# Performance work log

Hardware: AMD Instinct MI355X
Metric: run time of the kernel (lower is better)

The kernel has to match this reference:

```python
import jax, jax.numpy as jnp
import numpy as np

DIM = 512
QK_DIM = 128
B, N = 4, 4096
LN_EPS = 1e-5


def setup_inputs() -> dict:
    key = jax.random.key(0)
    ks = jax.random.split(key, 4)
    x = jax.random.normal(ks[0], (B, N, DIM), dtype=jnp.float32)
    ln_w = jnp.ones((DIM,), jnp.float32)
    ln_b = jnp.zeros((DIM,), jnp.float32)
    # Linear(dim -> qk_dim): torch default kaiming-uniform; small uniform is fine
    lim = 1.0 / np.sqrt(DIM)
    w_qk = jax.random.uniform(ks[1], (QK_DIM, DIM), jnp.float32, -lim, lim)
    b_qk = jax.random.uniform(ks[2], (QK_DIM,), jnp.float32, -lim, lim)
    # OffsetScale: gamma ~ N(0, 0.02), beta = 0, heads=2 (q, k)
    gamma = 0.02 * jax.random.normal(ks[3], (2, QK_DIM), jnp.float32)
    beta = jnp.zeros((2, QK_DIM), jnp.float32)
    return {"x": x, "ln_w": ln_w, "ln_b": ln_b, "w_qk": w_qk, "b_qk": b_qk, "gamma": gamma, "beta": beta}


def reference(x, ln_w, ln_b, w_qk, b_qk, gamma, beta):
    n = x.shape[-2]
    # LayerNorm over last dim
    mu = jnp.mean(x, axis=-1, keepdims=True)
    var = jnp.mean((x - mu) ** 2, axis=-1, keepdims=True)
    normed = (x - mu) * jax.lax.rsqrt(var + LN_EPS) * ln_w + ln_b
    # Linear + SiLU -> [b, n, qk_dim]
    qk = jax.nn.silu(jnp.einsum('bnd,ed->bne', normed, w_qk) + b_qk)
    # OffsetScale, heads=2 -> q, k
    q = qk * gamma[0] + beta[0]
    k = qk * gamma[1] + beta[1]
    # relu^2 row-normalized attention, [b, n, n]
    sim = jnp.einsum('bid,bjd->bij', q, k) / jnp.sqrt(jnp.float32(n))
    attn = jnp.square(jax.nn.relu(sim))
    attn = attn / (jnp.sum(attn, axis=-1, keepdims=True) + 1e-6)
    return attn
```

## Files before the change

kernel.cpp:

```cpp
#include <hip/hip_runtime.h>

#define DIM 512
#define QKD 128
#define BATCH 4
#define SEQ 4096

typedef __attribute__((ext_vector_type(8)))  _Float16 f16x8;
typedef __attribute__((ext_vector_type(4)))  _Float16 f16x4;
typedef __attribute__((ext_vector_type(4)))  float    f32x4;
typedef __attribute__((ext_vector_type(16))) float    f32x16;

__global__ __launch_bounds__(256) void wcvt_kernel(
    const float* __restrict__ w, _Float16* __restrict__ w16)
{
    const int i = (blockIdx.x * 256 + threadIdx.x) * 4;
    const float4 v = *(const float4*)(w + i);
    f16x4 o;
    o[0] = (_Float16)v.x; o[1] = (_Float16)v.y;
    o[2] = (_Float16)v.z; o[3] = (_Float16)v.w;
    *(f16x4*)(w16 + i) = o;
}

__global__ __launch_bounds__(256) void ln_qk_kernel(
    const float* __restrict__ x,
    const float* __restrict__ ln_w,
    const float* __restrict__ ln_b,
    const _Float16* __restrict__ w16,
    const float* __restrict__ b_qk,
    const float* __restrict__ gamma,
    const float* __restrict__ beta,
    _Float16* __restrict__ q_h,
    _Float16* __restrict__ k_h)
{
    __shared__ _Float16 As[32][520];
    const int tid  = threadIdx.x;
    const int wave = tid >> 6;
    const int lane = tid & 63;
    const int row0 = blockIdx.x * 32;

    float lw[8], lb[8];
    {
        const float4* w4 = (const float4*)ln_w;
        const float4* b4 = (const float4*)ln_b;
        float4 w0 = w4[lane * 2], w1 = w4[lane * 2 + 1];
        float4 b0 = b4[lane * 2], b1 = b4[lane * 2 + 1];
        lw[0]=w0.x; lw[1]=w0.y; lw[2]=w0.z; lw[3]=w0.w;
        lw[4]=w1.x; lw[5]=w1.y; lw[6]=w1.z; lw[7]=w1.w;
        lb[0]=b0.x; lb[1]=b0.y; lb[2]=b0.z; lb[3]=b0.w;
        lb[4]=b1.x; lb[5]=b1.y; lb[6]=b1.z; lb[7]=b1.w;
    }

    for (int rr = 0; rr < 8; ++rr) {
        const int r = wave * 8 + rr;
        const float4* xr = (const float4*)(x + (size_t)(row0 + r) * DIM);
        float4 v0 = xr[lane * 2], v1 = xr[lane * 2 + 1];
        float xv[8] = {v0.x, v0.y, v0.z, v0.w, v1.x, v1.y, v1.z, v1.w};
        float s = 0.f, s2 = 0.f;
#pragma unroll
        for (int j = 0; j < 8; ++j) { s += xv[j]; s2 = fmaf(xv[j], xv[j], s2); }
#pragma unroll
        for (int off = 32; off > 0; off >>= 1) {
            s  += __shfl_xor(s,  off);
            s2 += __shfl_xor(s2, off);
        }
        const float mu   = s * (1.f / DIM);
        const float var  = s2 * (1.f / DIM) - mu * mu;
        const float rstd = rsqrtf(var + 1e-5f);
        f16x8 hh;
#pragma unroll
        for (int j = 0; j < 8; ++j)
            hh[j] = (_Float16)(fmaf((xv[j] - mu) * rstd, lw[j], lb[j]));
        *(f16x8*)&As[r][lane * 8] = hh;
    }
    __syncthreads();

    const int mtile = wave & 1;
    const int nbase = (wave >> 1) * 64;
    const int lcol  = lane & 15;
    const int quad  = lane >> 4;

    f32x4 acc[4];
#pragma unroll
    for (int nt = 0; nt < 4; ++nt) acc[nt] = (f32x4){0.f, 0.f, 0.f, 0.f};

    const _Float16* arow = &As[mtile * 16 + lcol][quad * 8];
#pragma unroll 4
    for (int kc = 0; kc < 16; ++kc) {
        const f16x8 af = *(const f16x8*)(arow + kc * 32);
#pragma unroll
        for (int nt = 0; nt < 4; ++nt) {
            const int e = nbase + nt * 16 + lcol;
            const f16x8 bfr = *(const f16x8*)(w16 + (size_t)e * DIM + kc * 32 + quad * 8);
            acc[nt] = __builtin_amdgcn_mfma_f32_16x16x32_f16(af, bfr, acc[nt], 0, 0, 0);
        }
    }

    const size_t gbase = (size_t)blockIdx.x * 4096;
#pragma unroll
    for (int nt = 0; nt < 4; ++nt) {
        const int e = nbase + nt * 16 + lcol;
        const float bq  = b_qk[e];
        const float g0  = gamma[e]       * 0.125f;
        const float g1  = gamma[QKD + e] * 0.125f;
        const float be0 = beta[e]        * 0.125f;
        const float be1 = beta[QKD + e]  * 0.125f;
        const int eo = (e >> 3) * 256 + (e & 7);
#pragma unroll
        for (int reg = 0; reg < 4; ++reg) {
            const int m  = mtile * 16 + quad * 4 + reg;
            const float v   = acc[nt][reg] + bq;
            const float sil = v / (1.f + __expf(-v));
            const size_t off = gbase + (size_t)(eo + m * 8);
            q_h[off] = (_Float16)fmaf(sil, g0, be0);
            k_h[off] = (_Float16)fmaf(sil, g1, be1);
        }
    }
}

__global__ __launch_bounds__(256, 4) void rowsum_kernel(
    const _Float16* __restrict__ q_h,
    const _Float16* __restrict__ k_h,
    float* __restrict__ rsum)
{
    const int l     = blockIdx.x;
    const int batch = (l & 7) >> 1;
    const int chunk = ((l & 1) << 1) | ((l >> 3) & 1);
    const int tile  = l >> 4;
    const int r0    = tile * 32;

    const int wid  = threadIdx.x >> 6;
    const int lane = threadIdx.x & 63;
    const int n    = lane & 31;
    const int h    = lane >> 5;

    const _Float16* qb = q_h + (size_t)(batch * 128 + tile) * 4096;
    f16x8 aq[8];
#pragma unroll
    for (int kc = 0; kc < 8; ++kc)
        aq[kc] = *(const f16x8*)(qb + kc * 512 + lane * 8);

    const _Float16* kb0 = k_h + (size_t)(batch * 128 + chunk * 32 + wid) * 4096
                              + lane * 8;

    __shared__ float partial[4][32];

    float rs[16];
#pragma unroll
    for (int r = 0; r < 16; ++r) rs[r] = 0.f;

#pragma unroll 2
    for (int ct = 0; ct < 8; ++ct) {
        const _Float16* cb = kb0 + (size_t)(ct * 4) * 4096;
        f16x8 bf[8];
#pragma unroll
        for (int kc = 0; kc < 8; ++kc) bf[kc] = *(const f16x8*)(cb + kc * 512);

        f32x16 acc;
#pragma unroll
        for (int r = 0; r < 16; ++r) acc[r] = 0.f;
        __builtin_amdgcn_s_setprio(1);
#pragma unroll
        for (int kc = 0; kc < 8; ++kc)
            acc = __builtin_amdgcn_mfma_f32_32x32x16_f16(aq[kc], bf[kc], acc, 0, 0, 0);
        __builtin_amdgcn_s_setprio(0);
#pragma unroll
        for (int r = 0; r < 16; ++r) {
            const float t = fmaxf(acc[r], 0.f);
            rs[r] = fmaf(t, t, rs[r]);
        }
    }

#pragma unroll
    for (int r = 0; r < 16; ++r) {
        float v = rs[r];
        v += __shfl_xor(v, 1);
        v += __shfl_xor(v, 2);
        v += __shfl_xor(v, 4);
        v += __shfl_xor(v, 8);
        v += __shfl_xor(v, 16);
        if (n == 0) partial[wid][(r & 3) + 8 * (r >> 2) + 4 * h] = v;
    }
    __syncthreads();
    if (threadIdx.x < 32) {
        const float t = partial[0][threadIdx.x] + partial[1][threadIdx.x]
                      + partial[2][threadIdx.x] + partial[3][threadIdx.x];
        rsum[((size_t)batch * 4 + chunk) * SEQ + r0 + threadIdx.x] = t;
    }
}

__global__ __launch_bounds__(256, 4) void attn_norm_kernel(
    const _Float16* __restrict__ q_h,
    const _Float16* __restrict__ k_h,
    const float* __restrict__ rsum,
    float* __restrict__ out)
{
    const int l     = blockIdx.x;
    const int batch = (l & 7) >> 1;
    const int chunk = ((l & 1) << 1) | ((l >> 3) & 1);
    const int tile  = l >> 4;
    const int r0    = tile * 32;
    const int c0    = chunk * 1024;

    const int wid  = threadIdx.x >> 6;
    const int lane = threadIdx.x & 63;
    const int n    = lane & 31;
    const int h    = lane >> 5;

    const _Float16* qb = q_h + (size_t)(batch * 128 + tile) * 4096;
    f16x8 aq[8];
#pragma unroll
    for (int kc = 0; kc < 8; ++kc)
        aq[kc] = *(const f16x8*)(qb + kc * 512 + lane * 8);

    __shared__ float srow_s[32];
    if (threadIdx.x < 32) {
        const size_t base = (size_t)batch * 4 * SEQ + r0 + threadIdx.x;
        const float t = rsum[base] + rsum[base + SEQ]
                      + rsum[base + 2 * SEQ] + rsum[base + 3 * SEQ];
        srow_s[threadIdx.x] = rsqrtf(t + 1e-6f);
    }
    __syncthreads();

    float srow[16];
#pragma unroll
    for (int r = 0; r < 16; ++r)
        srow[r] = srow_s[(r & 3) + 8 * (r >> 2) + 4 * h];

    const _Float16* kb0 = k_h + (size_t)(batch * 128 + chunk * 32 + wid) * 4096
                              + lane * 8;
    float* ob = out + ((size_t)batch * SEQ + r0) * SEQ;

#pragma unroll 2
    for (int ct = 0; ct < 8; ++ct) {
        const _Float16* cb = kb0 + (size_t)(ct * 4) * 4096;
        f16x8 bf[8];
#pragma unroll
        for (int kc = 0; kc < 8; ++kc) bf[kc] = *(const f16x8*)(cb + kc * 512);

        f32x16 acc;
#pragma unroll
        for (int r = 0; r < 16; ++r) acc[r] = 0.f;
        __builtin_amdgcn_s_setprio(1);
#pragma unroll
        for (int kc = 0; kc < 8; ++kc)
            acc = __builtin_amdgcn_mfma_f32_32x32x16_f16(aq[kc], bf[kc], acc, 0, 0, 0);
        __builtin_amdgcn_s_setprio(0);

        const int col = c0 + ct * 128 + wid * 32 + n;
#pragma unroll
        for (int r = 0; r < 16; ++r) {
            const float t   = fmaxf(acc[r], 0.f) * srow[r];
            const int   row = (r & 3) + 8 * (r >> 2) + 4 * h;
            __builtin_nontemporal_store(t * t, ob + (size_t)row * SEQ + col);
        }
    }
}

extern "C" void kernel_launch(void* const* d_in, const int* in_sizes, int n_in,
                              void* d_out, int out_size, void* d_ws, size_t ws_size,
                              hipStream_t stream) {
    const float* x     = (const float*)d_in[0];
    const float* ln_w  = (const float*)d_in[1];
    const float* ln_b  = (const float*)d_in[2];
    const float* w_qk  = (const float*)d_in[3];
    const float* b_qk  = (const float*)d_in[4];
    const float* gamma = (const float*)d_in[5];
    const float* beta  = (const float*)d_in[6];
    float* out = (float*)d_out;

    _Float16* q_h = (_Float16*)d_ws;
    _Float16* k_h = q_h + (size_t)BATCH * SEQ * QKD;
    _Float16* w16 = k_h + (size_t)BATCH * SEQ * QKD;
    float*    rsum = (float*)(w16 + (size_t)QKD * DIM);

    hipLaunchKernelGGL(wcvt_kernel, dim3(64), dim3(256), 0, stream, w_qk, w16);
    hipLaunchKernelGGL(ln_qk_kernel, dim3((BATCH * SEQ) / 32), dim3(256), 0, stream,
                       x, ln_w, ln_b, w16, b_qk, gamma, beta, q_h, k_h);
    hipLaunchKernelGGL(rowsum_kernel, dim3(2048), dim3(256), 0, stream,
                       q_h, k_h, rsum);
    hipLaunchKernelGGL(attn_norm_kernel, dim3(2048), dim3(256), 0, stream,
                       q_h, k_h, rsum, out);
}
```

Before: 346.8 us.

## Pre-swizzle fp16 weights into MFMA fragment order and double row tile per block

The weight conversion kernel now writes w_qk in the exact per-lane MFMA B-fragment order, so ln_qk loads each fragment as one contiguous 16-byte read per lane instead of strided rows. The rowsum and attention-normalisation kernels move to 512-thread blocks covering 64 rows, with two row groups of waves sharing the same K column tiles. This is meant to reuse K loads across more rows and halve the block count. It raises per-block resources and halves the grid, which could reduce occupancy or load balance.

```diff
diff --git a/kernel.cpp b/kernel.cpp
--- a/kernel.cpp
+++ b/kernel.cpp
@@ -11,21 +11,29 @@
 typedef __attribute__((ext_vector_type(16))) float    f32x16;
 
 __global__ __launch_bounds__(256) void wcvt_kernel(
-    const float* __restrict__ w, _Float16* __restrict__ w16)
-{
-    const int i = (blockIdx.x * 256 + threadIdx.x) * 4;
-    const float4 v = *(const float4*)(w + i);
-    f16x4 o;
-    o[0] = (_Float16)v.x; o[1] = (_Float16)v.y;
-    o[2] = (_Float16)v.z; o[3] = (_Float16)v.w;
-    *(f16x4*)(w16 + i) = o;
+    const float* __restrict__ w, _Float16* __restrict__ w16f)
+{
+    const int t    = blockIdx.x * 256 + threadIdx.x;
+    const int lane = t & 63;
+    const int nb   = (t >> 6) & 7;
+    const int kc   = t >> 9;
+    const int e    = nb * 16 + (lane & 15);
+    const int d0   = kc * 32 + (lane >> 4) * 8;
+    const float4* src = (const float4*)(w + (size_t)e * DIM + d0);
+    const float4 a = src[0], b = src[1];
+    f16x8 o;
+    o[0] = (_Float16)a.x; o[1] = (_Float16)a.y;
+    o[2] = (_Float16)a.z; o[3] = (_Float16)a.w;
+    o[4] = (_Float16)b.x; o[5] = (_Float16)b.y;
+    o[6] = (_Float16)b.z; o[7] = (_Float16)b.w;
+    *(f16x8*)(w16f + (size_t)t * 8) = o;
 }
 
 __global__ __launch_bounds__(256) void ln_qk_kernel(
     const float* __restrict__ x,
     const float* __restrict__ ln_w,
     const float* __restrict__ ln_b,
-    const _Float16* __restrict__ w16,
+    const _Float16* __restrict__ w16f,
     const float* __restrict__ b_qk,
     const float* __restrict__ gamma,
     const float* __restrict__ beta,
@@ -75,7 +83,7 @@
     __syncthreads();
 
     const int mtile = wave & 1;
-    const int nbase = (wave >> 1) * 64;
+    const int nb0   = (wave >> 1) * 4;
     const int lcol  = lane & 15;
     const int quad  = lane >> 4;
 
@@ -89,8 +97,8 @@
         const f16x8 af = *(const f16x8*)(arow + kc * 32);
 #pragma unroll
         for (int nt = 0; nt < 4; ++nt) {
-            const int e = nbase + nt * 16 + lcol;
-            const f16x8 bfr = *(const f16x8*)(w16 + (size_t)e * DIM + kc * 32 + quad * 8);
+            const f16x8 bfr = *(const f16x8*)(
+                w16f + (size_t)((kc * 8 + nb0 + nt) * 64 + lane) * 8);
             acc[nt] = __builtin_amdgcn_mfma_f32_16x16x32_f16(af, bfr, acc[nt], 0, 0, 0);
         }
     }
@@ -98,7 +106,7 @@
     const size_t gbase = (size_t)blockIdx.x * 4096;
 #pragma unroll
     for (int nt = 0; nt < 4; ++nt) {
-        const int e = nbase + nt * 16 + lcol;
+        const int e = (nb0 + nt) * 16 + lcol;
         const float bq  = b_qk[e];
         const float g0  = gamma[e]       * 0.125f;
         const float g1  = gamma[QKD + e] * 0.125f;
@@ -117,7 +125,7 @@
     }
 }
 
-__global__ __launch_bounds__(256, 4) void rowsum_kernel(
+__global__ __launch_bounds__(512, 4) void rowsum_kernel(
     const _Float16* __restrict__ q_h,
     const _Float16* __restrict__ k_h,
     float* __restrict__ rsum)
@@ -126,23 +134,24 @@
     const int batch = (l & 7) >> 1;
     const int chunk = ((l & 1) << 1) | ((l >> 3) & 1);
     const int tile  = l >> 4;
-    const int r0    = tile * 32;
-
-    const int wid  = threadIdx.x >> 6;
-    const int lane = threadIdx.x & 63;
-    const int n    = lane & 31;
-    const int h    = lane >> 5;
-
-    const _Float16* qb = q_h + (size_t)(batch * 128 + tile) * 4096;
+
+    const int wid    = threadIdx.x >> 6;
+    const int rowblk = wid >> 2;
+    const int colw   = wid & 3;
+    const int lane   = threadIdx.x & 63;
+    const int n      = lane & 31;
+    const int h      = lane >> 5;
+
+    const _Float16* qb = q_h + (size_t)(batch * 128 + tile * 2 + rowblk) * 4096;
     f16x8 aq[8];
 #pragma unroll
     for (int kc = 0; kc < 8; ++kc)
         aq[kc] = *(const f16x8*)(qb + kc * 512 + lane * 8);
 
-    const _Float16* kb0 = k_h + (size_t)(batch * 128 + chunk * 32 + wid) * 4096
+    const _Float16* kb0 = k_h + (size_t)(batch * 128 + chunk * 32 + colw) * 4096
                               + lane * 8;
 
-    __shared__ float partial[4][32];
+    __shared__ float partial[8][32];
 
     float rs[16];
 #pragma unroll
@@ -181,14 +190,16 @@
         if (n == 0) partial[wid][(r & 3) + 8 * (r >> 2) + 4 * h] = v;
     }
     __syncthreads();
-    if (threadIdx.x < 32) {
-        const float t = partial[0][threadIdx.x] + partial[1][threadIdx.x]
-                      + partial[2][threadIdx.x] + partial[3][threadIdx.x];
-        rsum[((size_t)batch * 4 + chunk) * SEQ + r0 + threadIdx.x] = t;
-    }
-}
-
-__global__ __launch_bounds__(256, 4) void attn_norm_kernel(
+    if (threadIdx.x < 64) {
+        const int rb  = threadIdx.x >> 5;
+        const int idx = threadIdx.x & 31;
+        const float t = partial[rb * 4 + 0][idx] + partial[rb * 4 + 1][idx]
+                      + partial[rb * 4 + 2][idx] + partial[rb * 4 + 3][idx];
+        rsum[((size_t)batch * 4 + chunk) * SEQ + tile * 64 + rb * 32 + idx] = t;
+    }
+}
+
+__global__ __launch_bounds__(512, 4) void attn_norm_kernel(
     const _Float16* __restrict__ q_h,
     const _Float16* __restrict__ k_h,
     const float* __restrict__ rsum,
@@ -198,23 +209,24 @@
     const int batch = (l & 7) >> 1;
     const int chunk = ((l & 1) << 1) | ((l >> 3) & 1);
     const int tile  = l >> 4;
-    const int r0    = tile * 32;
     const int c0    = chunk * 1024;
 
-    const int wid  = threadIdx.x >> 6;
-    const int lane = threadIdx.x & 63;
-    const int n    = lane & 31;
-    const int h    = lane >> 5;
-
-    const _Float16* qb = q_h + (size_t)(batch * 128 + tile) * 4096;
+    const int wid    = threadIdx.x >> 6;
+    const int rowblk = wid >> 2;
+    const int colw   = wid & 3;
+    const int lane   = threadIdx.x & 63;
+    const int n      = lane & 31;
+    const int h      = lane >> 5;
+
+    const _Float16* qb = q_h + (size_t)(batch * 128 + tile * 2 + rowblk) * 4096;
     f16x8 aq[8];
 #pragma unroll
     for (int kc = 0; kc < 8; ++kc)
         aq[kc] = *(const f16x8*)(qb + kc * 512 + lane * 8);
 
-    __shared__ float srow_s[32];
-    if (threadIdx.x < 32) {
-        const size_t base = (size_t)batch * 4 * SEQ + r0 + threadIdx.x;
+    __shared__ float srow_s[64];
+    if (threadIdx.x < 64) {
+        const size_t base = (size_t)batch * 4 * SEQ + tile * 64 + threadIdx.x;
         const float t = rsum[base] + rsum[base + SEQ]
                       + rsum[base + 2 * SEQ] + rsum[base + 3 * SEQ];
         srow_s[threadIdx.x] = rsqrtf(t + 1e-6f);
@@ -224,11 +236,11 @@
     float srow[16];
 #pragma unroll
     for (int r = 0; r < 16; ++r)
-        srow[r] = srow_s[(r & 3) + 8 * (r >> 2) + 4 * h];
-
-    const _Float16* kb0 = k_h + (size_t)(batch * 128 + chunk * 32 + wid) * 4096
+        srow[r] = srow_s[rowblk * 32 + (r & 3) + 8 * (r >> 2) + 4 * h];
+
+    const _Float16* kb0 = k_h + (size_t)(batch * 128 + chunk * 32 + colw) * 4096
                               + lane * 8;
-    float* ob = out + ((size_t)batch * SEQ + r0) * SEQ;
+    float* ob = out + ((size_t)batch * SEQ + tile * 64 + rowblk * 32) * SEQ;
 
 #pragma unroll 2
     for (int ct = 0; ct < 8; ++ct) {
@@ -246,7 +258,7 @@
             acc = __builtin_amdgcn_mfma_f32_32x32x16_f16(aq[kc], bf[kc], acc, 0, 0, 0);
         __builtin_amdgcn_s_setprio(0);
 
-        const int col = c0 + ct * 128 + wid * 32 + n;
+        const int col = c0 + ct * 128 + colw * 32 + n;
 #pragma unroll
         for (int r = 0; r < 16; ++r) {
             const float t   = fmaxf(acc[r], 0.f) * srow[r];
@@ -268,16 +280,16 @@
     const float* beta  = (const float*)d_in[6];
     float* out = (float*)d_out;
 
-    _Float16* q_h = (_Float16*)d_ws;
-    _Float16* k_h = q_h + (size_t)BATCH * SEQ * QKD;
-    _Float16* w16 = k_h + (size_t)BATCH * SEQ * QKD;
-    float*    rsum = (float*)(w16 + (size_t)QKD * DIM);
-
-    hipLaunchKernelGGL(wcvt_kernel, dim3(64), dim3(256), 0, stream, w_qk, w16);
+    _Float16* q_h  = (_Float16*)d_ws;
+    _Float16* k_h  = q_h + (size_t)BATCH * SEQ * QKD;
+    _Float16* w16f = k_h + (size_t)BATCH * SEQ * QKD;
+    float*    rsum = (float*)(w16f + (size_t)QKD * DIM);
+
+    hipLaunchKernelGGL(wcvt_kernel, dim3(32), dim3(256), 0, stream, w_qk, w16f);
     hipLaunchKernelGGL(ln_qk_kernel, dim3((BATCH * SEQ) / 32), dim3(256), 0, stream,
-                       x, ln_w, ln_b, w16, b_qk, gamma, beta, q_h, k_h);
-    hipLaunchKernelGGL(rowsum_kernel, dim3(2048), dim3(256), 0, stream,
+                       x, ln_w, ln_b, w16f, b_qk, gamma, beta, q_h, k_h);
+    hipLaunchKernelGGL(rowsum_kernel, dim3(1024), dim3(512), 0, stream,
                        q_h, k_h, rsum);
-    hipLaunchKernelGGL(attn_norm_kernel, dim3(2048), dim3(256), 0, stream,
+    hipLaunchKernelGGL(attn_norm_kernel, dim3(1024), dim3(512), 0, stream,
                        q_h, k_h, rsum, out);
 }
```

After: 342.0 us. No clear change (-1.4%).
